# Optimization experiments

Measured on AMD Instinct MI355X. Metric: run time of the kernel, lower is better.

The kernel has to match this reference:

```python
import jax, jax.numpy as jnp
import numpy as np

ALPHA = 0.2        # LeakyReLU slope
THRESH = 0.01      # sparsity threshold


def setup_inputs() -> dict:
    key = jax.random.key(0)
    ks = jax.random.split(key, 5)
    B, T, F = 32, 128, 32          # batch, seq_len, input_size
    H, HD = 4, 16                  # heads, head_output_size (output_size=64)
    K = 2                          # Chebyshev order
    rank = min(16, F // 2)         # = 16
    x = jax.random.normal(ks[0], (B, T, F), jnp.float32)
    weight = jax.random.normal(ks[1], (K, H, F, HD), jnp.float32) * (1.0 / np.sqrt(F))
    bias = jnp.zeros((H * HD,), jnp.float32)
    temporal_query = jax.random.normal(ks[2], (H, HD), jnp.float32) * 0.1
    temporal_key = jax.random.normal(ks[3], (H, HD), jnp.float32) * 0.1
    feature_factor = jax.random.normal(ks[4], (H, 2, F, rank), jnp.float32) * 0.1
    return dict(x=x, weight=weight, bias=bias, temporal_query=temporal_query,
                temporal_key=temporal_key, feature_factor=feature_factor)


def reference(x, weight, bias, temporal_query, temporal_key, feature_factor):
    # Eval mode (dropout off). k=2: Chebyshev polynomials are [I, L_scaled].
    B, T, F = x.shape
    n = T * F
    x_flat = x.reshape(B, n)
    eye_T = jnp.eye(T, dtype=x.dtype)
    eye_F = jnp.eye(F, dtype=x.dtype)
    eye_n = jnp.eye(n, dtype=x.dtype)
    H = weight.shape[1]
    outs = []
    for h in range(H):
        # --- feature attention (low-rank), softmax over axis 1, threshold ---
        U = feature_factor[h, 0]               # [F, rank]
        V = feature_factor[h, 1]               # [F, rank]
        fa = jax.nn.softmax(jax.nn.leaky_relu(U @ V.T, ALPHA), axis=1)   # [F, F]
        # off-diagonal entries above threshold enter the graph (f1 != f2)
        fa = jnp.where((fa > THRESH) & ~jnp.eye(F, dtype=bool), fa, 0.0)
        # --- temporal attention on x projected by weight[0, h] ---
        xp = x @ weight[0, h]                  # [B, T, HD]
        q = xp @ temporal_query[h][:, None]    # [B, T, 1]
        kk = xp @ temporal_key[h][:, None]     # [B, T, 1]
        tl = jax.nn.leaky_relu(q + jnp.swapaxes(kk, 1, 2), ALPHA).mean(axis=0)  # [T, T]
        ta = jax.nn.softmax(tl, axis=1)
        ta = jnp.where((ta > THRESH) & ~jnp.eye(T, dtype=bool), ta, 0.0)
        # --- sparse graph (Kronecker structure) + self loops ---
        # temporal edges: A[t1*F+f, t2*F+f] = ta[t1,t2] -> kron(ta, I_F)
        # feature edges:  A[t*F+f1, t*F+f2] = fa[f1,f2] -> kron(I_T, fa)
        adj = jnp.kron(ta, eye_F) + jnp.kron(eye_T, fa) + eye_n   # [n, n]
        # --- normalized Laplacian ---
        d_inv_sqrt = (adj.sum(axis=1) + 1e-10) ** -0.5
        L = eye_n - d_inv_sqrt[:, None] * adj * d_inv_sqrt[None, :]
        # --- spectral-norm estimate via 3-step power iteration (no grad) ---
        v = jax.random.normal(jax.random.fold_in(jax.random.key(42), h), (n, 1), x.dtype)
        for _ in range(3):
            v = L @ v
            v = v / (jnp.linalg.norm(v) + 1e-10)
        sn = jnp.maximum(jnp.abs((v.T @ (L @ v))[0, 0]), 1.0)
        sn = jax.lax.stop_gradient(sn)
        L_scaled = 2.0 * L / sn - eye_n
        # --- Chebyshev conv, k=0 filter is identity, k=1 is L_scaled ---
        h0 = x @ weight[0, h]                                    # [B, T, HD]
        h1 = (x_flat @ L_scaled).reshape(B, T, F) @ weight[1, h]  # [B, T, HD]
        outs.append(h0 + h1)
    return jnp.concatenate(outs, axis=2) + bias
```

## Files before the change

kernel.cpp:

```cpp
#include <hip/hip_runtime.h>
#include <cstdint>

static constexpr int Bc = 32, Tc = 128, Fc = 32, Hc = 4, HDc = 16, RKc = 16;
static constexpr int Nc = Tc * Fc;
static constexpr int WS36 = 36;
static constexpr int XLS = 33;

__device__ __forceinline__ uint32_t rotl32(uint32_t v, int r) {
  return (v << r) | (v >> (32 - r));
}

__device__ __forceinline__ void threefry2x32(uint32_t k0, uint32_t k1,
                                             uint32_t& x0, uint32_t& x1) {
  uint32_t k2 = k0 ^ k1 ^ 0x1BD11BDAu;
  x0 += k0; x1 += k1;
#define TF_R(r) { x0 += x1; x1 = rotl32(x1, (r)); x1 ^= x0; }
  TF_R(13) TF_R(15) TF_R(26) TF_R(6)
  x0 += k1; x1 += k2 + 1u;
  TF_R(17) TF_R(29) TF_R(16) TF_R(24)
  x0 += k2; x1 += k0 + 2u;
  TF_R(13) TF_R(15) TF_R(26) TF_R(6)
  x0 += k0; x1 += k1 + 3u;
  TF_R(17) TF_R(29) TF_R(16) TF_R(24)
  x0 += k1; x1 += k2 + 4u;
  TF_R(13) TF_R(15) TF_R(26) TF_R(6)
  x0 += k2; x1 += k0 + 5u;
#undef TF_R
}

__device__ __forceinline__ float erfinv_f32(float x) {
  float w = -__logf((1.0f - x) * (1.0f + x));
  float p;
  if (w < 5.0f) {
    w -= 2.5f;
    p = 2.81022636e-08f;
    p = fmaf(p, w, 3.43273939e-07f);
    p = fmaf(p, w, -3.5233877e-06f);
    p = fmaf(p, w, -4.39150654e-06f);
    p = fmaf(p, w, 0.00021858087f);
    p = fmaf(p, w, -0.00125372503f);
    p = fmaf(p, w, -0.00417768164f);
    p = fmaf(p, w, 0.246640727f);
    p = fmaf(p, w, 1.50140941f);
  } else {
    w = sqrtf(w) - 3.0f;
    p = -0.000200214257f;
    p = fmaf(p, w, 0.000100950558f);
    p = fmaf(p, w, 0.00134934322f);
    p = fmaf(p, w, -0.00367342844f);
    p = fmaf(p, w, 0.00573950773f);
    p = fmaf(p, w, -0.0076224613f);
    p = fmaf(p, w, 0.00943887047f);
    p = fmaf(p, w, 1.00167406f);
    p = fmaf(p, w, 2.83297682f);
  }
  return p * x;
}

__device__ __forceinline__ float jax_normal_from_bits(uint32_t bits) {
  const float lo = -0.99999994f;
  float f = __uint_as_float((bits >> 9) | 0x3f800000u) - 1.0f;
  float u = fmaxf(lo, f * 2.0f + lo);
  return 1.41421354f * erfinv_f32(u);
}

__global__ __launch_bounds__(256)
void proj_kernel(const float* __restrict__ x, const float* __restrict__ weight,
                 const float* __restrict__ tqg, const float* __restrict__ tkg,
                 float* __restrict__ ws_q, float* __restrict__ ws_k) {
  const int b = blockIdx.x;
  const int tid = (int)threadIdx.x;
  __shared__ float xL[Tc * XLS];
  __shared__ float wqS[Hc * Fc], wkS[Hc * Fc];

  const float* xb = x + (size_t)b * Nc;
  for (int j = tid; j < Nc / 4; j += 256) {
    int row = j >> 3, c4 = j & 7;
    float4 v = *(const float4*)&xb[row * Fc + 4 * c4];
    xL[row * XLS + 4 * c4 + 0] = v.x;
    xL[row * XLS + 4 * c4 + 1] = v.y;
    xL[row * XLS + 4 * c4 + 2] = v.z;
    xL[row * XLS + 4 * c4 + 3] = v.w;
  }
  if (tid < Hc * Fc) {
    int h = tid >> 5, f = tid & 31;
    const float* W0 = weight + h * (Fc * HDc) + f * HDc;
    float aq = 0.f, ak = 0.f;
    for (int d = 0; d < HDc; ++d) {
      aq += W0[d] * tqg[h * HDc + d];
      ak += W0[d] * tkg[h * HDc + d];
    }
    wqS[tid] = aq; wkS[tid] = ak;
  }
  __syncthreads();

  const int h = tid >> 6, lane = tid & 63;
#pragma unroll
  for (int half = 0; half < 2; ++half) {
    int t = lane + 64 * half;
    float aq = 0.f, ak = 0.f;
    for (int f = 0; f < Fc; ++f) {
      float xv = xL[t * XLS + f];
      aq += xv * wqS[h * Fc + f];
      ak += xv * wkS[h * Fc + f];
    }
    ws_q[h * Nc + b * Tc + t] = aq;
    ws_k[h * Nc + b * Tc + t] = ak;
  }
}

__global__ __launch_bounds__(256)
void score_kernel(const float* __restrict__ ws_q, const float* __restrict__ ws_k,
                  float* __restrict__ ws_ta, float* __restrict__ ws_rs) {
  const int h = blockIdx.x, chunk = blockIdx.y;
  const int tid = (int)threadIdx.x;
  __shared__ float kS[Bc * Tc];
  __shared__ float qS[Bc * 4];

  for (int j = tid; j < Bc * Tc / 4; j += 256)
    ((float4*)kS)[j] = ((const float4*)(ws_k + (size_t)h * Nc))[j];
  if (tid < Bc * 4) {
    int b = tid >> 2, r = tid & 3;
    qS[tid] = ws_q[(size_t)h * Nc + b * Tc + 4 * chunk + r];
  }
  __syncthreads();

  const int r = tid >> 6, lane = tid & 63;
  const int gr = 4 * chunk + r;
  float acc0 = 0.f, acc1 = 0.f;
  for (int b = 0; b < Bc; ++b) {
    float q = qS[b * 4 + r];
    float k0 = kS[b * Tc + lane];
    float k1 = kS[b * Tc + lane + 64];
    float s0 = q + k0, s1 = q + k1;
    acc0 += fmaxf(s0, 0.2f * s0);
    acc1 += fmaxf(s1, 0.2f * s1);
  }
  acc0 *= (1.0f / 32.0f);
  acc1 *= (1.0f / 32.0f);

  float m = fmaxf(acc0, acc1);
  for (int o = 32; o > 0; o >>= 1) m = fmaxf(m, __shfl_xor(m, o, 64));
  float e0 = expf(acc0 - m), e1 = expf(acc1 - m);
  float se = e0 + e1;
  for (int o = 32; o > 0; o >>= 1) se += __shfl_xor(se, o, 64);
  float p0 = e0 / se, p1 = e1 / se;
  p0 = ((p0 > 0.01f) && (lane != gr)) ? p0 : 0.f;
  p1 = ((p1 > 0.01f) && (lane + 64 != gr)) ? p1 : 0.f;
  float rs = p0 + p1;
  for (int o = 32; o > 0; o >>= 1) rs += __shfl_xor(rs, o, 64);

  float* tar = ws_ta + (size_t)h * (Tc * Tc) + (size_t)gr * Tc;
  tar[lane] = p0;
  tar[lane + 64] = p1;
  if (lane == 0) ws_rs[h * Tc + gr] = rs;
}

__global__ __launch_bounds__(512, 1)
void conv_kernel(const float* __restrict__ x, const float* __restrict__ weight,
                 const float* __restrict__ bias, const float* __restrict__ ffg,
                 const float* __restrict__ ws_ta, const float* __restrict__ ws_rs,
                 float* __restrict__ out) {
  const int b = blockIdx.x, h = blockIdx.y;
  const int tid = (int)threadIdx.x;
  const int lane = tid & 63, wvi = tid >> 6;

  __shared__ __align__(16) float faS[Fc * WS36];
  __shared__ __align__(16) float faTS[Fc * WS36];
  __shared__ __align__(16) float W0s[Fc * HDc];
  __shared__ __align__(16) float W1s[Fc * HDc];
  __shared__ __align__(16) float vtmp[Nc];
  __shared__ __align__(16) float wbuf[Tc * WS36];
  __shared__ float rsT[Tc], rsF[Fc];
  __shared__ float red[8][2];
  __shared__ int flagS;

  const int t = tid >> 2, fq = tid & 3, f0 = 8 * fq;

  if (tid < Tc) rsT[tid] = ws_rs[h * Tc + tid];
  {
    W0s[tid] = weight[h * (Fc * HDc) + tid];
    W1s[tid] = weight[(Hc + h) * (Fc * HDc) + tid];
  }
  if (tid < 64) {
    int nz = (ws_rs[h * Tc + tid] > 0.f) || (ws_rs[h * Tc + tid + 64] > 0.f);
    unsigned long long bal = __ballot(nz);
    if (tid == 0) flagS = (bal != 0ull) ? 1 : 0;
  }
  const float* xb = x + (size_t)b * Nc;
  float4 xva = *(const float4*)&xb[t * Fc + f0];
  float4 xvb = *(const float4*)&xb[t * Fc + f0 + 4];

  for (int j2 = tid; j2 < Fc * Fc; j2 += 512) {
    const float* U = ffg + h * (2 * Fc * RKc);
    const float* V = U + Fc * RKc;
    int f1 = j2 >> 5, f2 = j2 & 31;
    float acc = 0.f;
    for (int r = 0; r < RKc; ++r) acc += U[f1 * RKc + r] * V[f2 * RKc + r];
    float val = fmaxf(acc, 0.2f * acc);
    float m = val;
    for (int o = 16; o > 0; o >>= 1) m = fmaxf(m, __shfl_xor(m, o, 32));
    float e = expf(val - m), se = e;
    for (int o = 16; o > 0; o >>= 1) se += __shfl_xor(se, o, 32);
    float pv = e / se;
    pv = (pv > 0.01f && f1 != f2) ? pv : 0.f;
    faS[f1 * WS36 + f2] = pv;
    faTS[f2 * WS36 + f1] = pv;
    float rsum = pv;
    for (int o = 16; o > 0; o >>= 1) rsum += __shfl_xor(rsum, o, 32);
    if (f2 == 0) rsF[f1] = rsum;
  }
  {
    uint32_t fk0 = 0u, fk1 = (uint32_t)h;
    threefry2x32(0u, 42u, fk0, fk1);
    float n0[4], n1[4];
#pragma unroll
    for (int jj = 0; jj < 4; ++jj) {
      int l = tid * 4 + jj;
      uint32_t c0 = (uint32_t)l, c1 = (uint32_t)(l + 2048);
      threefry2x32(fk0, fk1, c0, c1);
      n0[jj] = jax_normal_from_bits(c0);
      n1[jj] = jax_normal_from_bits(c1);
    }
    *(float4*)&vtmp[tid * 4]        = make_float4(n0[0], n0[1], n0[2], n0[3]);
    *(float4*)&vtmp[2048 + tid * 4] = make_float4(n1[0], n1[1], n1[2], n1[3]);
  }
  __syncthreads();

  float s_reg[8], v[8];
  {
    float rrow = rsT[t];
#pragma unroll
    for (int j = 0; j < 8; ++j)
      s_reg[j] = 1.0f / sqrtf(rrow + rsF[f0 + j] + 1.0f + 1e-10f);
    float4 v0a = *(const float4*)&vtmp[t * Fc + f0];
    float4 v0b = *(const float4*)&vtmp[t * Fc + f0 + 4];
    v[0]=v0a.x; v[1]=v0a.y; v[2]=v0a.z; v[3]=v0a.w;
    v[4]=v0b.x; v[5]=v0b.y; v[6]=v0b.z; v[7]=v0b.w;
  }

  const int srcBase = lane & 60;
  float u4[8];
  for (int it = 0; it < 4; ++it) {
    float w[8];
#pragma unroll
    for (int j = 0; j < 8; ++j) w[j] = s_reg[j] * v[j];
    if (flagS) {
      *(float4*)&wbuf[t * WS36 + f0]     = make_float4(w[0], w[1], w[2], w[3]);
      *(float4*)&wbuf[t * WS36 + f0 + 4] = make_float4(w[4], w[5], w[6], w[7]);
      __syncthreads();
    }
    float wrow[32];
#pragma unroll
    for (int oq = 0; oq < 4; ++oq)
#pragma unroll
      for (int j = 0; j < 8; ++j)
        wrow[oq * 8 + j] = __shfl(w[j], srcBase + oq, 64);
    float acc[8] = {};
#pragma unroll
    for (int f2 = 0; f2 < Fc; ++f2) {
      float4 fa0 = *(const float4*)&faTS[f2 * WS36 + f0];
      float4 fa1 = *(const float4*)&faTS[f2 * WS36 + f0 + 4];
      float ww = wrow[f2];
      acc[0] += ww * fa0.x; acc[1] += ww * fa0.y;
      acc[2] += ww * fa0.z; acc[3] += ww * fa0.w;
      acc[4] += ww * fa1.x; acc[5] += ww * fa1.y;
      acc[6] += ww * fa1.z; acc[7] += ww * fa1.w;
    }
    if (flagS) {
      const float* taG = ws_ta + (size_t)h * (Tc * Tc) + (size_t)t * Tc;
      for (int k = 0; k < Tc; ++k) {
        float tak = taG[k];
        float4 w0 = *(const float4*)&wbuf[k * WS36 + f0];
        float4 w1 = *(const float4*)&wbuf[k * WS36 + f0 + 4];
        acc[0] += tak * w0.x; acc[1] += tak * w0.y;
        acc[2] += tak * w0.z; acc[3] += tak * w0.w;
        acc[4] += tak * w1.x; acc[5] += tak * w1.y;
        acc[6] += tak * w1.z; acc[7] += tak * w1.w;
      }
      __syncthreads();
    }
    float nv[8];
#pragma unroll
    for (int j = 0; j < 8; ++j) {
      float a = acc[j] + w[j];
      nv[j] = v[j] - s_reg[j] * a;
    }
    if (it < 3) {
#pragma unroll
      for (int j = 0; j < 8; ++j) v[j] = nv[j];
    } else {
#pragma unroll
      for (int j = 0; j < 8; ++j) u4[j] = nv[j];
    }
  }
  {
    float pn = 0.f, pd = 0.f;
#pragma unroll
    for (int j = 0; j < 8; ++j) { pn += v[j] * u4[j]; pd += v[j] * v[j]; }
    for (int o = 32; o > 0; o >>= 1) {
      pn += __shfl_down(pn, o, 64);
      pd += __shfl_down(pd, o, 64);
    }
    if (lane == 0) { red[wvi][0] = pn; red[wvi][1] = pd; }
  }
  __syncthreads();
  float num = 0.f, den = 0.f;
#pragma unroll
  for (int i2 = 0; i2 < 8; ++i2) { num += red[i2][0]; den += red[i2][1]; }
  const float sn = fmaxf(fabsf(num / den), 1.0f);
  const float csn = 2.0f / sn;
  const float cm1 = csn - 1.0f;

  float X[8] = {xva.x, xva.y, xva.z, xva.w, xvb.x, xvb.y, xvb.z, xvb.w};
  float Z[8];
#pragma unroll
  for (int j = 0; j < 8; ++j) Z[j] = s_reg[j] * X[j];
  float gacc[8] = {};
  if (flagS) {
    *(float4*)&wbuf[t * WS36 + f0]     = make_float4(Z[0], Z[1], Z[2], Z[3]);
    *(float4*)&wbuf[t * WS36 + f0 + 4] = make_float4(Z[4], Z[5], Z[6], Z[7]);
    __syncthreads();
    const float* taG = ws_ta + (size_t)h * (Tc * Tc);
    for (int k = 0; k < Tc; ++k) {
      float tak = taG[(size_t)k * Tc + t];
      float4 z0 = *(const float4*)&wbuf[k * WS36 + f0];
      float4 z1 = *(const float4*)&wbuf[k * WS36 + f0 + 4];
      gacc[0] += tak * z0.x; gacc[1] += tak * z0.y;
      gacc[2] += tak * z0.z; gacc[3] += tak * z0.w;
      gacc[4] += tak * z1.x; gacc[5] += tak * z1.y;
      gacc[6] += tak * z1.z; gacc[7] += tak * z1.w;
    }
  }
  {
    float zrow[32];
#pragma unroll
    for (int oq = 0; oq < 4; ++oq)
#pragma unroll
      for (int j = 0; j < 8; ++j)
        zrow[oq * 8 + j] = __shfl(Z[j], srcBase + oq, 64);
#pragma unroll
    for (int f2 = 0; f2 < Fc; ++f2) {
      float4 fa0 = *(const float4*)&faS[f2 * WS36 + f0];
      float4 fa1 = *(const float4*)&faS[f2 * WS36 + f0 + 4];
      float zz = zrow[f2];
      gacc[0] += zz * fa0.x; gacc[1] += zz * fa0.y;
      gacc[2] += zz * fa0.z; gacc[3] += zz * fa0.w;
      gacc[4] += zz * fa1.x; gacc[5] += zz * fa1.y;
      gacc[6] += zz * fa1.z; gacc[7] += zz * fa1.w;
    }
  }
  float G[8];
#pragma unroll
  for (int j = 0; j < 8; ++j)
    G[j] = cm1 * X[j] - csn * s_reg[j] * (gacc[j] + Z[j]);

  float acc2[16] = {};
#pragma unroll
  for (int jf = 0; jf < 8; ++jf) {
    int f = f0 + jf;
#pragma unroll
    for (int hq = 0; hq < 4; ++hq) {
      float4 w0 = *(const float4*)&W0s[f * HDc + 4 * hq];
      float4 w1 = *(const float4*)&W1s[f * HDc + 4 * hq];
      acc2[4*hq+0] += X[jf] * w0.x + G[jf] * w1.x;
      acc2[4*hq+1] += X[jf] * w0.y + G[jf] * w1.y;
      acc2[4*hq+2] += X[jf] * w0.z + G[jf] * w1.z;
      acc2[4*hq+3] += X[jf] * w0.w + G[jf] * w1.w;
    }
  }
#pragma unroll
  for (int i2 = 0; i2 < 16; ++i2) {
    acc2[i2] += __shfl_xor(acc2[i2], 1, 64);
    acc2[i2] += __shfl_xor(acc2[i2], 2, 64);
  }
  {
    float4 bv = *(const float4*)&bias[h * HDc + 4 * fq];
    float4 o4;
    if      (fq == 0) o4 = make_float4(acc2[0],  acc2[1],  acc2[2],  acc2[3]);
    else if (fq == 1) o4 = make_float4(acc2[4],  acc2[5],  acc2[6],  acc2[7]);
    else if (fq == 2) o4 = make_float4(acc2[8],  acc2[9],  acc2[10], acc2[11]);
    else              o4 = make_float4(acc2[12], acc2[13], acc2[14], acc2[15]);
    o4.x += bv.x; o4.y += bv.y; o4.z += bv.z; o4.w += bv.w;
    *(float4*)&out[((size_t)b * Tc + t) * (Hc * HDc) + h * HDc + 4 * fq] = o4;
  }
}

extern "C" void kernel_launch(void* const* d_in, const int* in_sizes, int n_in,
                              void* d_out, int out_size, void* d_ws, size_t ws_size,
                              hipStream_t stream) {
  const float* x      = (const float*)d_in[0];
  const float* weight = (const float*)d_in[1];
  const float* bias   = (const float*)d_in[2];
  const float* tqg    = (const float*)d_in[3];
  const float* tkg    = (const float*)d_in[4];
  const float* ffg    = (const float*)d_in[5];
  float* out = (float*)d_out;

  float* ws = (float*)d_ws;
  float* ws_ta = ws;
  float* ws_rs = ws + 65536;
  float* ws_q  = ws + 66048;
  float* ws_k  = ws + 82432;

  proj_kernel<<<dim3(Bc), dim3(256), 0, stream>>>(
      x, weight, tqg, tkg, ws_q, ws_k);
  score_kernel<<<dim3(Hc, 32), dim3(256), 0, stream>>>(
      ws_q, ws_k, ws_ta, ws_rs);
  conv_kernel<<<dim3(Bc, Hc), dim3(512), 0, stream>>>(
      x, weight, bias, ffg, ws_ta, ws_rs, out);
}
```

Before: 34.52 us.

## Split per-head graph setup and power iteration into separate head kernel

The feature-attention softmax, RNG vector and 3-step power iteration for the spectral norm depended only on the head but were recomputed by every (batch, head) block of the conv kernel. They now run once per head in a new 4-block head_kernel that writes fa, row sums and sn to workspace, and conv_kernel just loads them. proj_kernel also uses 512 threads, one output per thread. The redundant work across 32 batch blocks goes away, at the cost of one more launch and a serial 4-block stage with little parallelism.

```diff
diff --git a/kernel.cpp b/kernel.cpp
--- a/kernel.cpp
+++ b/kernel.cpp
@@ -64,7 +64,7 @@
   return 1.41421354f * erfinv_f32(u);
 }
 
-__global__ __launch_bounds__(256)
+__global__ __launch_bounds__(512)
 void proj_kernel(const float* __restrict__ x, const float* __restrict__ weight,
                  const float* __restrict__ tqg, const float* __restrict__ tkg,
                  float* __restrict__ ws_q, float* __restrict__ ws_k) {
@@ -74,7 +74,7 @@
   __shared__ float wqS[Hc * Fc], wkS[Hc * Fc];
 
   const float* xb = x + (size_t)b * Nc;
-  for (int j = tid; j < Nc / 4; j += 256) {
+  for (int j = tid; j < Nc / 4; j += 512) {
     int row = j >> 3, c4 = j & 7;
     float4 v = *(const float4*)&xb[row * Fc + 4 * c4];
     xL[row * XLS + 4 * c4 + 0] = v.x;
@@ -94,19 +94,15 @@
   }
   __syncthreads();
 
-  const int h = tid >> 6, lane = tid & 63;
-#pragma unroll
-  for (int half = 0; half < 2; ++half) {
-    int t = lane + 64 * half;
-    float aq = 0.f, ak = 0.f;
-    for (int f = 0; f < Fc; ++f) {
-      float xv = xL[t * XLS + f];
-      aq += xv * wqS[h * Fc + f];
-      ak += xv * wkS[h * Fc + f];
-    }
-    ws_q[h * Nc + b * Tc + t] = aq;
-    ws_k[h * Nc + b * Tc + t] = ak;
-  }
+  const int t = tid & 127, h = tid >> 7;
+  float aq = 0.f, ak = 0.f;
+  for (int f = 0; f < Fc; ++f) {
+    float xv = xL[t * XLS + f];
+    aq += xv * wqS[h * Fc + f];
+    ak += xv * wkS[h * Fc + f];
+  }
+  ws_q[h * Nc + b * Tc + t] = aq;
+  ws_k[h * Nc + b * Tc + t] = ak;
 }
 
 __global__ __launch_bounds__(256)
@@ -157,18 +153,14 @@
 }
 
 __global__ __launch_bounds__(512, 1)
-void conv_kernel(const float* __restrict__ x, const float* __restrict__ weight,
-                 const float* __restrict__ bias, const float* __restrict__ ffg,
-                 const float* __restrict__ ws_ta, const float* __restrict__ ws_rs,
-                 float* __restrict__ out) {
-  const int b = blockIdx.x, h = blockIdx.y;
+void head_kernel(const float* __restrict__ ffg, const float* __restrict__ ws_ta,
+                 const float* __restrict__ ws_rs, float* __restrict__ ws_fa,
+                 float* __restrict__ ws_rsF, float* __restrict__ ws_sn) {
+  const int h = blockIdx.x;
   const int tid = (int)threadIdx.x;
   const int lane = tid & 63, wvi = tid >> 6;
 
-  __shared__ __align__(16) float faS[Fc * WS36];
   __shared__ __align__(16) float faTS[Fc * WS36];
-  __shared__ __align__(16) float W0s[Fc * HDc];
-  __shared__ __align__(16) float W1s[Fc * HDc];
   __shared__ __align__(16) float vtmp[Nc];
   __shared__ __align__(16) float wbuf[Tc * WS36];
   __shared__ float rsT[Tc], rsF[Fc];
@@ -178,19 +170,11 @@
   const int t = tid >> 2, fq = tid & 3, f0 = 8 * fq;
 
   if (tid < Tc) rsT[tid] = ws_rs[h * Tc + tid];
-  {
-    W0s[tid] = weight[h * (Fc * HDc) + tid];
-    W1s[tid] = weight[(Hc + h) * (Fc * HDc) + tid];
-  }
   if (tid < 64) {
     int nz = (ws_rs[h * Tc + tid] > 0.f) || (ws_rs[h * Tc + tid + 64] > 0.f);
     unsigned long long bal = __ballot(nz);
     if (tid == 0) flagS = (bal != 0ull) ? 1 : 0;
   }
-  const float* xb = x + (size_t)b * Nc;
-  float4 xva = *(const float4*)&xb[t * Fc + f0];
-  float4 xvb = *(const float4*)&xb[t * Fc + f0 + 4];
-
   for (int j2 = tid; j2 < Fc * Fc; j2 += 512) {
     const float* U = ffg + h * (2 * Fc * RKc);
     const float* V = U + Fc * RKc;
@@ -204,11 +188,11 @@
     for (int o = 16; o > 0; o >>= 1) se += __shfl_xor(se, o, 32);
     float pv = e / se;
     pv = (pv > 0.01f && f1 != f2) ? pv : 0.f;
-    faS[f1 * WS36 + f2] = pv;
     faTS[f2 * WS36 + f1] = pv;
+    ws_fa[h * (Fc * Fc) + j2] = pv;
     float rsum = pv;
     for (int o = 16; o > 0; o >>= 1) rsum += __shfl_xor(rsum, o, 32);
-    if (f2 == 0) rsF[f1] = rsum;
+    if (f2 == 0) { rsF[f1] = rsum; ws_rsF[h * Fc + f1] = rsum; }
   }
   {
     uint32_t fk0 = 0u, fk1 = (uint32_t)h;
@@ -305,17 +289,65 @@
     if (lane == 0) { red[wvi][0] = pn; red[wvi][1] = pd; }
   }
   __syncthreads();
-  float num = 0.f, den = 0.f;
-#pragma unroll
-  for (int i2 = 0; i2 < 8; ++i2) { num += red[i2][0]; den += red[i2][1]; }
-  const float sn = fmaxf(fabsf(num / den), 1.0f);
+  if (tid == 0) {
+    float num = 0.f, den = 0.f;
+    for (int i2 = 0; i2 < 8; ++i2) { num += red[i2][0]; den += red[i2][1]; }
+    ws_sn[h] = fmaxf(fabsf(num / den), 1.0f);
+  }
+}
+
+__global__ __launch_bounds__(512, 1)
+void conv_kernel(const float* __restrict__ x, const float* __restrict__ weight,
+                 const float* __restrict__ bias, const float* __restrict__ ws_ta,
+                 const float* __restrict__ ws_rs, const float* __restrict__ ws_fa,
+                 const float* __restrict__ ws_rsF, const float* __restrict__ ws_sn,
+                 float* __restrict__ out) {
+  const int b = blockIdx.x, h = blockIdx.y;
+  const int tid = (int)threadIdx.x;
+  const int lane = tid & 63;
+
+  __shared__ __align__(16) float faS[Fc * WS36];
+  __shared__ __align__(16) float W0s[Fc * HDc];
+  __shared__ __align__(16) float W1s[Fc * HDc];
+  __shared__ __align__(16) float wbuf[Tc * WS36];
+  __shared__ float rsT[Tc], rsF[Fc];
+  __shared__ int flagS;
+
+  const int t = tid >> 2, fq = tid & 3, f0 = 8 * fq;
+
+  if (tid < Tc) rsT[tid] = ws_rs[h * Tc + tid];
+  if (tid < Fc) rsF[tid] = ws_rsF[h * Fc + tid];
+  {
+    W0s[tid] = weight[h * (Fc * HDc) + tid];
+    W1s[tid] = weight[(Hc + h) * (Fc * HDc) + tid];
+  }
+  for (int i = tid; i < Fc * Fc; i += 512)
+    faS[(i >> 5) * WS36 + (i & 31)] = ws_fa[h * (Fc * Fc) + i];
+  if (tid < 64) {
+    int nz = (ws_rs[h * Tc + tid] > 0.f) || (ws_rs[h * Tc + tid + 64] > 0.f);
+    unsigned long long bal = __ballot(nz);
+    if (tid == 0) flagS = (bal != 0ull) ? 1 : 0;
+  }
+  const float* xb = x + (size_t)b * Nc;
+  float4 xva = *(const float4*)&xb[t * Fc + f0];
+  float4 xvb = *(const float4*)&xb[t * Fc + f0 + 4];
+  const float sn = ws_sn[h];
   const float csn = 2.0f / sn;
   const float cm1 = csn - 1.0f;
-
+  __syncthreads();
+
+  float s_reg[8];
+  {
+    float rrow = rsT[t];
+#pragma unroll
+    for (int j = 0; j < 8; ++j)
+      s_reg[j] = 1.0f / sqrtf(rrow + rsF[f0 + j] + 1.0f + 1e-10f);
+  }
   float X[8] = {xva.x, xva.y, xva.z, xva.w, xvb.x, xvb.y, xvb.z, xvb.w};
   float Z[8];
 #pragma unroll
   for (int j = 0; j < 8; ++j) Z[j] = s_reg[j] * X[j];
+
   float gacc[8] = {};
   if (flagS) {
     *(float4*)&wbuf[t * WS36 + f0]     = make_float4(Z[0], Z[1], Z[2], Z[3]);
@@ -333,6 +365,7 @@
     }
   }
   {
+    const int srcBase = lane & 60;
     float zrow[32];
 #pragma unroll
     for (int oq = 0; oq < 4; ++oq)
@@ -398,15 +431,20 @@
   float* out = (float*)d_out;
 
   float* ws = (float*)d_ws;
-  float* ws_ta = ws;
-  float* ws_rs = ws + 65536;
-  float* ws_q  = ws + 66048;
-  float* ws_k  = ws + 82432;
-
-  proj_kernel<<<dim3(Bc), dim3(256), 0, stream>>>(
+  float* ws_ta  = ws;
+  float* ws_rs  = ws + 65536;
+  float* ws_q   = ws + 66048;
+  float* ws_k   = ws + 82432;
+  float* ws_fa  = ws + 98816;
+  float* ws_rsF = ws + 102912;
+  float* ws_sn  = ws + 103040;
+
+  proj_kernel<<<dim3(Bc), dim3(512), 0, stream>>>(
       x, weight, tqg, tkg, ws_q, ws_k);
   score_kernel<<<dim3(Hc, 32), dim3(256), 0, stream>>>(
       ws_q, ws_k, ws_ta, ws_rs);
+  head_kernel<<<dim3(Hc), dim3(512), 0, stream>>>(
+      ffg, ws_ta, ws_rs, ws_fa, ws_rsF, ws_sn);
   conv_kernel<<<dim3(Bc, Hc), dim3(512), 0, stream>>>(
-      x, weight, bias, ffg, ws_ta, ws_rs, out);
-}
+      x, weight, bias, ws_ta, ws_rs, ws_fa, ws_rsF, ws_sn, out);
+}
```

New measurement: 37.35 us. +8.2%, slower.
